# Kernel optimization log

Measured on AMD Instinct MI355X. Metric: run time of the kernel, lower is better.

Reference implementation:

```python
import jax, jax.numpy as jnp
import numpy as np

N_WAY = 5
NKPTS = 17
EMBED = 512
N_SUPPORT = 25  # 5-way 5-shot
N_QUERY = 65536


def setup_inputs() -> dict:
    key = jax.random.key(0)
    ks = jax.random.split(key, 12)
    def lin(k, fan_in, fan_out):
        return jax.random.normal(k, (fan_in, fan_out), jnp.float32) / np.float32(np.sqrt(fan_in))
    return {
        'support_features': jax.random.normal(ks[0], (1, N_SUPPORT, EMBED), jnp.float32),
        'support_keypoints': jax.random.uniform(ks[1], (N_SUPPORT, NKPTS, 2), jnp.float32),
        'query_features': jax.random.normal(ks[2], (N_QUERY, EMBED), jnp.float32),
        'image_coords': jax.random.uniform(ks[3], (N_QUERY, 2), jnp.float32) * 512.0,
        'W1': lin(ks[4], EMBED, EMBED), 'b1': jnp.zeros((EMBED,), jnp.float32),
        'W2': lin(ks[5], EMBED, EMBED), 'b2': jnp.zeros((EMBED,), jnp.float32),
        'Wo1': lin(ks[6], EMBED, EMBED // 2), 'bo1': jnp.zeros((EMBED // 2,), jnp.float32),
        'Wo2': lin(ks[7], EMBED // 2, 2), 'bo2': jnp.zeros((2,), jnp.float32),
        'Wc1': lin(ks[8], EMBED, EMBED // 2), 'bc1': jnp.zeros((EMBED // 2,), jnp.float32),
        'Wc2': lin(ks[9], EMBED // 2, 1), 'bc2': jnp.zeros((1,), jnp.float32),
        'temperature': jnp.float32(1.0),
    }


def reference(support_features, support_keypoints, query_features, image_coords,
              W1, b1, W2, b2, Wo1, bo1, Wo2, bo2, Wc1, bc1, Wc2, bc2, temperature):
    eps = 1e-8
    nkpts = support_keypoints.shape[1]
    n_query = query_features.shape[0]
    D = query_features.shape[-1]

    # --- compute_prototypes (batch_size == 1; per-kpt prototype identical by construction) ---
    sf = support_features.reshape(-1, D)                      # [Ns, D]
    h = jnp.maximum(sf @ W1 + b1, 0.0) @ W2 + b2              # prototype_net MLP
    n_per = h.shape[0] // N_WAY
    proto_way = h.reshape(N_WAY, n_per, D).mean(axis=1)       # [n_way, D]
    prototypes = jnp.broadcast_to(proto_way[:, None, :], (N_WAY, nkpts, D))

    # --- compute_distances: 1 - cosine_sim, scaled by temperature ---
    qn = jnp.linalg.norm(query_features, axis=-1)             # [Nq]
    pn = jnp.linalg.norm(proto_way, axis=-1)                  # [n_way]
    sim = (query_features @ proto_way.T) / jnp.maximum(qn[:, None] * pn[None, :], eps)
    dist_way = (1.0 - sim) / temperature                      # [Nq, n_way]
    distances = jnp.broadcast_to(dist_way[:, :, None], (n_query, N_WAY, nkpts))

    # --- predict_keypoints ---
    # avg over kpts is a no-op (identical per kpt); argmin over ways
    class_predictions = jnp.argmin(dist_way, axis=1)          # [Nq] int
    # softmax over a single scalar == 1.0, so keypoints == offset broadcast over kpts
    offset = jnp.maximum(query_features @ Wo1 + bo1, 0.0) @ Wo2 + bo2   # [Nq, 2]
    conf = jax.nn.sigmoid(jnp.maximum(query_features @ Wc1 + bc1, 0.0) @ Wc2 + bc2)  # [Nq, 1]
    keypoints = jnp.broadcast_to(offset[:, None, :], (n_query, nkpts, 2))
    keypoints = jax.nn.sigmoid(keypoints) * image_coords[:, None, :]    # image_coords provided
    confidence = jnp.broadcast_to(conf, (n_query, nkpts))

    return keypoints, confidence, distances, class_predictions, prototypes
```

## Files before the change

kernel.cpp:

```cpp
#include <hip/hip_runtime.h>
#include <hip/hip_bf16.h>

#define NQ 65536
#define DIM 512
#define HID 256
#define NWAY 5
#define NKPTS 17

typedef short bf16x8 __attribute__((ext_vector_type(8)));
typedef float f32x4 __attribute__((ext_vector_type(4)));
typedef _Float16 half8 __attribute__((ext_vector_type(8)));

static __device__ __forceinline__ unsigned short f2bf(float f) {
    unsigned int x = __float_as_uint(f);
    unsigned int r = (x + 0x7fffu + ((x >> 16) & 1u)) >> 16;
    return (unsigned short)r;
}

__global__ __launch_bounds__(256) void k_sup1(const float* __restrict__ sf,
                                              const float* __restrict__ W1, const float* __restrict__ b1,
                                              float* __restrict__ ws_h1) {
    int w = blockIdx.x * 4 + (threadIdx.x >> 6);
    int lane = threadIdx.x & 63;
    int s = w >> 9;
    int c = w & 511;
    const float* ip = sf + s * DIM + lane * 8;
    float4 a0 = *(const float4*)ip;
    float4 a1 = *(const float4*)(ip + 4);
    float av[8] = {a0.x, a0.y, a0.z, a0.w, a1.x, a1.y, a1.z, a1.w};
    float acc = 0.0f;
    #pragma unroll
    for (int j = 0; j < 8; j++)
        acc += av[j] * W1[(lane * 8 + j) * DIM + c];
    #pragma unroll
    for (int off = 32; off > 0; off >>= 1)
        acc += __shfl_xor(acc, off, 64);
    if (lane == 0)
        ws_h1[s * DIM + c] = fmaxf(acc + b1[c], 0.0f);
}

__global__ __launch_bounds__(256) void k_mid(const float* __restrict__ ws_h1,
                                             const float* __restrict__ W2, const float* __restrict__ b2,
                                             const float* __restrict__ Wo1, const float* __restrict__ Wc1,
                                             float* __restrict__ ws_proto, unsigned short* __restrict__ wb) {
    int bx = blockIdx.x;
    int t = threadIdx.x;
    if (bx < 640) {
        int g = bx * 4 + (t >> 6);
        int lane = t & 63;
        int w = g >> 9;
        int c = g & 511;
        const float* base = ws_h1 + (w * 5) * DIM + lane * 8;
        float av[8] = {0, 0, 0, 0, 0, 0, 0, 0};
        #pragma unroll
        for (int s = 0; s < 5; s++) {
            float4 x0 = *(const float4*)(base + s * DIM);
            float4 x1 = *(const float4*)(base + s * DIM + 4);
            av[0] += x0.x; av[1] += x0.y; av[2] += x0.z; av[3] += x0.w;
            av[4] += x1.x; av[5] += x1.y; av[6] += x1.z; av[7] += x1.w;
        }
        float acc = 0.0f;
        #pragma unroll
        for (int j = 0; j < 8; j++)
            acc += (av[j] * 0.2f) * W2[(lane * 8 + j) * DIM + c];
        #pragma unroll
        for (int off = 32; off > 0; off >>= 1)
            acc += __shfl_xor(acc, off, 64);
        if (lane == 0)
            ws_proto[w * DIM + c] = acc + b2[c];
    } else {
        __shared__ unsigned short T[64][72];
        int tb = bx - 640;
        const float* src = (tb < 32) ? Wo1 : Wc1;
        int cofs = (tb < 32) ? 0 : 256;
        int tt = tb & 31;
        int kt = tt >> 2;
        int ct = tt & 3;
        int i = t >> 2;
        int qd = t & 3;
        const float* rp = src + (size_t)(kt * 64 + i) * HID + ct * 64 + qd * 16;
        #pragma unroll
        for (int v = 0; v < 4; v++) {
            float4 x = *(const float4*)(rp + v * 4);
            T[qd * 16 + v * 4 + 0][i] = f2bf(x.x);
            T[qd * 16 + v * 4 + 1][i] = f2bf(x.y);
            T[qd * 16 + v * 4 + 2][i] = f2bf(x.z);
            T[qd * 16 + v * 4 + 3][i] = f2bf(x.w);
        }
        __syncthreads();
        int j = t >> 2;
        int part = t & 3;
        uint4 o0 = *(const uint4*)&T[j][part * 16];
        uint4 o1 = *(const uint4*)&T[j][part * 16 + 8];
        unsigned short* dst = wb + (size_t)(cofs + ct * 64 + j) * DIM + kt * 64 + part * 16;
        *(uint4*)dst = o0;
        *(uint4*)(dst + 8) = o1;
    }
}

__global__ __launch_bounds__(256) void k_fused(const float* __restrict__ qf, const unsigned short* __restrict__ wb,
                                               const float* __restrict__ ws_proto,
                                               const float* __restrict__ temp_p,
                                               const float* __restrict__ bo1, const float* __restrict__ Wo2,
                                               const float* __restrict__ bo2,
                                               const float* __restrict__ bc1, const float* __restrict__ Wc2,
                                               const float* __restrict__ bc2,
                                               const float* __restrict__ ic,
                                               float* __restrict__ out_kp, float* __restrict__ out_conf,
                                               float* __restrict__ out_dist, float* __restrict__ out_class,
                                               float* __restrict__ out_proto) {
    __shared__ __align__(16) char smem[37376];
    unsigned short* Alds = (unsigned short*)smem;
    unsigned short* Blds = (unsigned short*)(smem + 5120);
    float* s_proto = (float*)(smem + 25600);
    float* dlds = (float*)(smem + 35840);
    float* pn_lds = (float*)(smem + 37120);
    _Float16* hlds = (_Float16*)smem;
    float* offlds = (float*)(smem + 33792);

    int bx = blockIdx.x;
    int mb = bx >> 1;
    int nb = bx & 1;
    int t = threadIdx.x;
    int wv = t >> 6;
    int lane = t & 63;
    int r = lane & 15;
    int q8 = (lane >> 4) * 8;

    if (bx < 85 && t < 128) {
        f32x4 v = *(const f32x4*)(ws_proto + (bx / NKPTS) * DIM + t * 4);
        *(f32x4*)(out_proto + (size_t)bx * DIM + t * 4) = v;
    }

    f32x4 acc[4][4];
    #pragma unroll
    for (int i = 0; i < 4; i++)
        #pragma unroll
        for (int j = 0; j < 4; j++) {
            f32x4 z = {0.0f, 0.0f, 0.0f, 0.0f};
            acc[i][j] = z;
        }

    int am = t >> 2;
    int akc = t & 3;
    int mine = ((t >> 7) == nb);
    const float* aptr = qf + ((size_t)(mb * 64 + am)) * DIM + akc * 8;
    const unsigned short* bptr = wb + ((size_t)(nb * 256 + t)) * DIM;

    for (int i = t; i < NWAY * DIM; i += 256) s_proto[i] = ws_proto[i];

    float ds[NWAY] = {0, 0, 0, 0, 0};
    float qq = 0.0f;

    float4 A0 = *(const float4*)(aptr);
    float4 A1 = *(const float4*)(aptr + 4);
    uint4 B0 = *(const uint4*)(bptr);
    uint4 B1 = *(const uint4*)(bptr + 8);
    uint4 B2 = *(const uint4*)(bptr + 16);
    uint4 B3 = *(const uint4*)(bptr + 24);

    for (int it = 0; it < 16; it++) {
        unsigned int p0 = f2bf(A0.x) | ((unsigned int)f2bf(A0.y) << 16);
        unsigned int p1 = f2bf(A0.z) | ((unsigned int)f2bf(A0.w) << 16);
        unsigned int p2 = f2bf(A1.x) | ((unsigned int)f2bf(A1.y) << 16);
        unsigned int p3 = f2bf(A1.z) | ((unsigned int)f2bf(A1.w) << 16);
        float av[8] = {A0.x, A0.y, A0.z, A0.w, A1.x, A1.y, A1.z, A1.w};
        __syncthreads();
        *(uint4*)(Alds + am * 40 + akc * 8) = make_uint4(p0, p1, p2, p3);
        *(uint4*)(Blds + t * 40) = B0;
        *(uint4*)(Blds + t * 40 + 8) = B1;
        *(uint4*)(Blds + t * 40 + 16) = B2;
        *(uint4*)(Blds + t * 40 + 24) = B3;
        __syncthreads();
        if (it < 15) {
            int k1 = (it + 1) * 32;
            A0 = *(const float4*)(aptr + k1);
            A1 = *(const float4*)(aptr + k1 + 4);
            B0 = *(const uint4*)(bptr + k1);
            B1 = *(const uint4*)(bptr + k1 + 8);
            B2 = *(const uint4*)(bptr + k1 + 16);
            B3 = *(const uint4*)(bptr + k1 + 24);
        }
        if (mine) {
            int kb = it * 32 + akc * 8;
            #pragma unroll
            for (int w = 0; w < NWAY; w++) {
                f32x4 pv0 = *(const f32x4*)(s_proto + w * DIM + kb);
                f32x4 pv1 = *(const f32x4*)(s_proto + w * DIM + kb + 4);
                ds[w] += av[0] * pv0[0] + av[1] * pv0[1] + av[2] * pv0[2] + av[3] * pv0[3]
                       + av[4] * pv1[0] + av[5] * pv1[1] + av[6] * pv1[2] + av[7] * pv1[3];
            }
            #pragma unroll
            for (int j = 0; j < 8; j++) qq += av[j] * av[j];
        }
        bf16x8 af[4], bf[4];
        #pragma unroll
        for (int mt = 0; mt < 4; mt++)
            af[mt] = *(const bf16x8*)(Alds + (mt * 16 + r) * 40 + q8);
        #pragma unroll
        for (int nt = 0; nt < 4; nt++)
            bf[nt] = *(const bf16x8*)(Blds + (wv * 64 + nt * 16 + r) * 40 + q8);
        #pragma unroll
        for (int mt = 0; mt < 4; mt++)
            #pragma unroll
            for (int nt = 0; nt < 4; nt++)
                acc[mt][nt] = __builtin_amdgcn_mfma_f32_16x16x32_bf16(af[mt], bf[nt], acc[mt][nt], 0, 0, 0);
    }

    for (int w = wv; w < NWAY; w += 4) {
        f32x4 a = *(const f32x4*)(s_proto + w * DIM + lane * 8);
        f32x4 b = *(const f32x4*)(s_proto + w * DIM + lane * 8 + 4);
        float ss = a[0]*a[0] + a[1]*a[1] + a[2]*a[2] + a[3]*a[3]
                 + b[0]*b[0] + b[1]*b[1] + b[2]*b[2] + b[3]*b[3];
        #pragma unroll
        for (int off = 32; off > 0; off >>= 1) ss += __shfl_xor(ss, off, 64);
        if (lane == 0) pn_lds[w] = sqrtf(ss);
    }
    if (mine) {
        #pragma unroll
        for (int off = 1; off <= 2; off <<= 1) {
            #pragma unroll
            for (int w = 0; w < NWAY; w++) ds[w] += __shfl_xor(ds[w], off, 64);
            qq += __shfl_xor(qq, off, 64);
        }
    }
    __syncthreads();
    if (mine && akc == 0) {
        float qn = sqrtf(qq);
        float invt = 1.0f / temp_p[0];
        float mv = 1e30f;
        int ami = 0;
        #pragma unroll
        for (int w = 0; w < NWAY; w++) {
            float den = fmaxf(qn * pn_lds[w], 1e-8f);
            float d = (1.0f - ds[w] / den) * invt;
            dlds[am * 5 + w] = d;
            if (d < mv) { mv = d; ami = w; }
        }
        out_class[mb * 64 + am] = (float)ami;
    }
    __syncthreads();

    {
        int qlo = nb * 32;
        for (int i = t; i < 32 * NWAY * NKPTS; i += 256) {
            int q = qlo + i / (NWAY * NKPTS);
            int rem = i - (i / (NWAY * NKPTS)) * (NWAY * NKPTS);
            out_dist[(size_t)(mb * 64 + q) * (NWAY * NKPTS) + rem] = dlds[q * 5 + rem / NKPTS];
        }
    }

    const float* bias = nb ? bc1 : bo1;
    #pragma unroll
    for (int nt = 0; nt < 4; nt++) {
        int cl = wv * 64 + nt * 16 + r;
        float bv = bias[cl];
        #pragma unroll
        for (int mt = 0; mt < 4; mt++)
            #pragma unroll
            for (int rg = 0; rg < 4; rg++) {
                int ml = mt * 16 + (lane >> 4) * 4 + rg;
                float v = acc[mt][nt][rg] + bv;
                hlds[ml * 264 + cl] = (_Float16)fmaxf(v, 0.0f);
            }
    }
    __syncthreads();

    if (nb == 0) {
        if (t < 64) {
            float ox = bo2[0], oy = bo2[1];
            for (int c0 = 0; c0 < 256; c0 += 8) {
                half8 hv = *(const half8*)(hlds + t * 264 + c0);
                #pragma unroll
                for (int j = 0; j < 8; j++) {
                    float hf = (float)hv[j];
                    ox += hf * Wo2[(c0 + j) * 2];
                    oy += hf * Wo2[(c0 + j) * 2 + 1];
                }
            }
            offlds[t * 2] = ox;
            offlds[t * 2 + 1] = oy;
        }
        __syncthreads();
        for (int i = t; i < 64 * 34; i += 256) {
            int q = i / 34;
            int rem = i - q * 34;
            int j = rem & 1;
            size_t Q = (size_t)mb * 64 + q;
            float o = offlds[q * 2 + j];
            float sg = 1.0f / (1.0f + __expf(-o));
            out_kp[Q * 34 + rem] = sg * ic[Q * 2 + j];
        }
    } else {
        if (t < 64) {
            float cl2 = bc2[0];
            for (int c0 = 0; c0 < 256; c0 += 8) {
                half8 hv = *(const half8*)(hlds + t * 264 + c0);
                #pragma unroll
                for (int j = 0; j < 8; j++) cl2 += (float)hv[j] * Wc2[c0 + j];
            }
            offlds[t] = 1.0f / (1.0f + __expf(-cl2));
        }
        __syncthreads();
        for (int i = t; i < 64 * 17; i += 256) {
            int q = i / 17;
            out_conf[(size_t)mb * 64 * 17 + i] = offlds[q];
        }
    }
}

extern "C" void kernel_launch(void* const* d_in, const int* in_sizes, int n_in,
                              void* d_out, int out_size, void* d_ws, size_t ws_size,
                              hipStream_t stream) {
    const float* sf = (const float*)d_in[0];
    const float* qf = (const float*)d_in[2];
    const float* ic = (const float*)d_in[3];
    const float* W1 = (const float*)d_in[4];
    const float* b1 = (const float*)d_in[5];
    const float* W2 = (const float*)d_in[6];
    const float* b2 = (const float*)d_in[7];
    const float* Wo1 = (const float*)d_in[8];
    const float* bo1 = (const float*)d_in[9];
    const float* Wo2 = (const float*)d_in[10];
    const float* bo2 = (const float*)d_in[11];
    const float* Wc1 = (const float*)d_in[12];
    const float* bc1 = (const float*)d_in[13];
    const float* Wc2 = (const float*)d_in[14];
    const float* bc2 = (const float*)d_in[15];
    const float* temp = (const float*)d_in[16];

    float* out = (float*)d_out;
    float* out_kp = out;
    float* out_conf = out + 2228224;
    float* out_dist = out + 3342336;
    float* out_class = out + 8912896;
    float* out_proto = out + 8978432;

    char* ws = (char*)d_ws;
    float* ws_h1 = (float*)ws;
    float* ws_proto = (float*)(ws + 51200);
    unsigned short* ws_wb = (unsigned short*)(ws + 65536);

    hipLaunchKernelGGL(k_sup1, dim3(3200), dim3(256), 0, stream, sf, W1, b1, ws_h1);
    hipLaunchKernelGGL(k_mid, dim3(704), dim3(256), 0, stream, ws_h1, W2, b2, Wo1, Wc1, ws_proto, ws_wb);
    hipLaunchKernelGGL(k_fused, dim3(2048), dim3(256), 0, stream, qf, ws_wb, ws_proto, temp,
                       bo1, Wo2, bo2, bc1, Wc2, bc2, ic, out_kp, out_conf, out_dist, out_class, out_proto);
}
```

Measured before the change: 366.4 us.

## Split query prep from GEMM and use async LDS loads with larger tiles

Restructures the whole pipeline. The support MLP kernels now stage inputs in LDS and use fewer blocks. A new prep kernel converts the query features to bf16 in workspace and computes cosine distances and class predictions. A separate GEMM kernel uses 128x256 tiles with 512 threads, double-buffered global_load_lds copies and an XOR-swizzled LDS layout. The split avoids doing the distance math and bf16 conversion inside the GEMM loop, but adds an extra 64 MB bf16 write and read of the queries through HBM.

```diff
diff --git a/kernel.cpp b/kernel.cpp
--- a/kernel.cpp
+++ b/kernel.cpp
@@ -17,60 +17,69 @@
     return (unsigned short)r;
 }
 
-__global__ __launch_bounds__(256) void k_sup1(const float* __restrict__ sf,
-                                              const float* __restrict__ W1, const float* __restrict__ b1,
-                                              float* __restrict__ ws_h1) {
-    int w = blockIdx.x * 4 + (threadIdx.x >> 6);
-    int lane = threadIdx.x & 63;
-    int s = w >> 9;
-    int c = w & 511;
-    const float* ip = sf + s * DIM + lane * 8;
-    float4 a0 = *(const float4*)ip;
-    float4 a1 = *(const float4*)(ip + 4);
-    float av[8] = {a0.x, a0.y, a0.z, a0.w, a1.x, a1.y, a1.z, a1.w};
+static __device__ __forceinline__ void async16(void* l, const void* g) {
+    __builtin_amdgcn_global_load_lds(
+        (const __attribute__((address_space(1))) unsigned int*)g,
+        (__attribute__((address_space(3))) unsigned int*)l, 16, 0, 0);
+}
+
+__global__ __launch_bounds__(256) void k_sup(const float* __restrict__ sf,
+                                             const float* __restrict__ W1, const float* __restrict__ b1,
+                                             float* __restrict__ ws_h1) {
+    __shared__ float sfl[512];
+    __shared__ float red[4][64];
+    int bx = blockIdx.x;
+    int s = bx >> 3, cb = bx & 7;
+    int t = threadIdx.x;
+    if (t < 128) ((float4*)sfl)[t] = ((const float4*)(sf + s * DIM))[t];
+    __syncthreads();
+    int c = cb * 64 + (t & 63);
+    int qd = t >> 6;
+    const float* Wp = W1 + (size_t)qd * 128 * DIM + c;
     float acc = 0.0f;
-    #pragma unroll
-    for (int j = 0; j < 8; j++)
-        acc += av[j] * W1[(lane * 8 + j) * DIM + c];
-    #pragma unroll
-    for (int off = 32; off > 0; off >>= 1)
-        acc += __shfl_xor(acc, off, 64);
-    if (lane == 0)
-        ws_h1[s * DIM + c] = fmaxf(acc + b1[c], 0.0f);
-}
-
-__global__ __launch_bounds__(256) void k_mid(const float* __restrict__ ws_h1,
-                                             const float* __restrict__ W2, const float* __restrict__ b2,
-                                             const float* __restrict__ Wo1, const float* __restrict__ Wc1,
-                                             float* __restrict__ ws_proto, unsigned short* __restrict__ wb) {
+    #pragma unroll 4
+    for (int kk = 0; kk < 128; kk++)
+        acc += sfl[qd * 128 + kk] * Wp[(size_t)kk * DIM];
+    red[qd][t & 63] = acc;
+    __syncthreads();
+    if (t < 64) {
+        float h = red[0][t] + red[1][t] + red[2][t] + red[3][t] + b1[cb * 64 + t];
+        ws_h1[s * DIM + cb * 64 + t] = fmaxf(h, 0.0f);
+    }
+}
+
+__global__ __launch_bounds__(256) void k_mid2(const float* __restrict__ ws_h1,
+                                              const float* __restrict__ W2, const float* __restrict__ b2,
+                                              const float* __restrict__ Wo1, const float* __restrict__ Wc1,
+                                              float* __restrict__ ws_proto, unsigned short* __restrict__ wb) {
     int bx = blockIdx.x;
     int t = threadIdx.x;
-    if (bx < 640) {
-        int g = bx * 4 + (t >> 6);
-        int lane = t & 63;
-        int w = g >> 9;
-        int c = g & 511;
-        const float* base = ws_h1 + (w * 5) * DIM + lane * 8;
-        float av[8] = {0, 0, 0, 0, 0, 0, 0, 0};
-        #pragma unroll
-        for (int s = 0; s < 5; s++) {
-            float4 x0 = *(const float4*)(base + s * DIM);
-            float4 x1 = *(const float4*)(base + s * DIM + 4);
-            av[0] += x0.x; av[1] += x0.y; av[2] += x0.z; av[3] += x0.w;
-            av[4] += x1.x; av[5] += x1.y; av[6] += x1.z; av[7] += x1.w;
-        }
+    if (bx < 40) {
+        __shared__ float ml[512];
+        __shared__ float red[4][64];
+        int w = bx >> 3, cb = bx & 7;
+        for (int i = t; i < 512; i += 256) {
+            float sum = 0.0f;
+            #pragma unroll
+            for (int s5 = 0; s5 < 5; s5++) sum += ws_h1[(w * 5 + s5) * DIM + i];
+            ml[i] = sum * 0.2f;
+        }
+        __syncthreads();
+        int c = cb * 64 + (t & 63);
+        int qd = t >> 6;
+        const float* Wp = W2 + (size_t)qd * 128 * DIM + c;
         float acc = 0.0f;
-        #pragma unroll
-        for (int j = 0; j < 8; j++)
-            acc += (av[j] * 0.2f) * W2[(lane * 8 + j) * DIM + c];
-        #pragma unroll
-        for (int off = 32; off > 0; off >>= 1)
-            acc += __shfl_xor(acc, off, 64);
-        if (lane == 0)
-            ws_proto[w * DIM + c] = acc + b2[c];
+        #pragma unroll 4
+        for (int kk = 0; kk < 128; kk++)
+            acc += ml[qd * 128 + kk] * Wp[(size_t)kk * DIM];
+        red[qd][t & 63] = acc;
+        __syncthreads();
+        if (t < 64)
+            ws_proto[w * DIM + cb * 64 + t] =
+                red[0][t] + red[1][t] + red[2][t] + red[3][t] + b2[cb * 64 + t];
     } else {
         __shared__ unsigned short T[64][72];
-        int tb = bx - 640;
+        int tb = bx - 40;
         const float* src = (tb < 32) ? Wo1 : Wc1;
         int cofs = (tb < 32) ? 0 : 256;
         int tt = tb & 31;
@@ -98,213 +107,259 @@
     }
 }
 
-__global__ __launch_bounds__(256) void k_fused(const float* __restrict__ qf, const unsigned short* __restrict__ wb,
-                                               const float* __restrict__ ws_proto,
-                                               const float* __restrict__ temp_p,
-                                               const float* __restrict__ bo1, const float* __restrict__ Wo2,
-                                               const float* __restrict__ bo2,
-                                               const float* __restrict__ bc1, const float* __restrict__ Wc2,
-                                               const float* __restrict__ bc2,
-                                               const float* __restrict__ ic,
-                                               float* __restrict__ out_kp, float* __restrict__ out_conf,
-                                               float* __restrict__ out_dist, float* __restrict__ out_class,
-                                               float* __restrict__ out_proto) {
-    __shared__ __align__(16) char smem[37376];
-    unsigned short* Alds = (unsigned short*)smem;
-    unsigned short* Blds = (unsigned short*)(smem + 5120);
-    float* s_proto = (float*)(smem + 25600);
-    float* dlds = (float*)(smem + 35840);
-    float* pn_lds = (float*)(smem + 37120);
-    _Float16* hlds = (_Float16*)smem;
-    float* offlds = (float*)(smem + 33792);
-
-    int bx = blockIdx.x;
-    int mb = bx >> 1;
-    int nb = bx & 1;
-    int t = threadIdx.x;
-    int wv = t >> 6;
-    int lane = t & 63;
-    int r = lane & 15;
-    int q8 = (lane >> 4) * 8;
-
-    if (bx < 85 && t < 128) {
+__global__ __launch_bounds__(256) void k_prep(const float* __restrict__ qf,
+                                              const float* __restrict__ ws_proto,
+                                              const float* __restrict__ temp_p,
+                                              unsigned short* __restrict__ qbf,
+                                              float* __restrict__ out_dist, float* __restrict__ out_class,
+                                              float* __restrict__ out_proto) {
+    __shared__ float dlds[32 * NWAY];
+    int bx = blockIdx.x, t = threadIdx.x;
+    int wv = t >> 6, lane = t & 63;
+
+    if (bx < NWAY * NKPTS && t < 128) {
         f32x4 v = *(const f32x4*)(ws_proto + (bx / NKPTS) * DIM + t * 4);
         *(f32x4*)(out_proto + (size_t)bx * DIM + t * 4) = v;
     }
 
+    float p[NWAY][8];
+    float pn[NWAY];
+    {
+        float pp[NWAY];
+        #pragma unroll
+        for (int w = 0; w < NWAY; w++) {
+            f32x4 a = *(const f32x4*)(ws_proto + w * DIM + lane * 8);
+            f32x4 b = *(const f32x4*)(ws_proto + w * DIM + lane * 8 + 4);
+            p[w][0] = a[0]; p[w][1] = a[1]; p[w][2] = a[2]; p[w][3] = a[3];
+            p[w][4] = b[0]; p[w][5] = b[1]; p[w][6] = b[2]; p[w][7] = b[3];
+            float s = 0.0f;
+            #pragma unroll
+            for (int j = 0; j < 8; j++) s += p[w][j] * p[w][j];
+            pp[w] = s;
+        }
+        #pragma unroll
+        for (int off = 32; off > 0; off >>= 1) {
+            #pragma unroll
+            for (int w = 0; w < NWAY; w++) pp[w] += __shfl_xor(pp[w], off, 64);
+        }
+        #pragma unroll
+        for (int w = 0; w < NWAY; w++) pn[w] = sqrtf(pp[w]);
+    }
+    float invt = 1.0f / temp_p[0];
+
+    int qbase = bx * 32 + wv * 8;
+    for (int qi = 0; qi < 8; qi++) {
+        int Q = qbase + qi;
+        const float* vp = qf + (size_t)Q * DIM + lane * 8;
+        float4 v0 = *(const float4*)vp;
+        float4 v1 = *(const float4*)(vp + 4);
+        unsigned int r0 = f2bf(v0.x) | ((unsigned int)f2bf(v0.y) << 16);
+        unsigned int r1 = f2bf(v0.z) | ((unsigned int)f2bf(v0.w) << 16);
+        unsigned int r2 = f2bf(v1.x) | ((unsigned int)f2bf(v1.y) << 16);
+        unsigned int r3 = f2bf(v1.z) | ((unsigned int)f2bf(v1.w) << 16);
+        *(uint4*)(qbf + (size_t)Q * DIM + lane * 8) = make_uint4(r0, r1, r2, r3);
+
+        float av[8] = {v0.x, v0.y, v0.z, v0.w, v1.x, v1.y, v1.z, v1.w};
+        float d[NWAY + 1];
+        #pragma unroll
+        for (int w = 0; w < NWAY; w++) {
+            float s = 0.0f;
+            #pragma unroll
+            for (int j = 0; j < 8; j++) s += av[j] * p[w][j];
+            d[w] = s;
+        }
+        {
+            float s = 0.0f;
+            #pragma unroll
+            for (int j = 0; j < 8; j++) s += av[j] * av[j];
+            d[NWAY] = s;
+        }
+        #pragma unroll
+        for (int off = 32; off > 0; off >>= 1) {
+            #pragma unroll
+            for (int k2 = 0; k2 < NWAY + 1; k2++) d[k2] += __shfl_xor(d[k2], off, 64);
+        }
+        float qn = sqrtf(d[NWAY]);
+        float mv = 1e30f; int ami = 0;
+        float d0, d1c, d2c, d3c, d4c;
+        {
+            float dist[NWAY];
+            #pragma unroll
+            for (int w = 0; w < NWAY; w++) {
+                float den = fmaxf(qn * pn[w], 1e-8f);
+                float dd = (1.0f - d[w] / den) * invt;
+                dist[w] = dd;
+                if (dd < mv) { mv = dd; ami = w; }
+            }
+            d0 = dist[0]; d1c = dist[1]; d2c = dist[2]; d3c = dist[3]; d4c = dist[4];
+        }
+        if (lane == 0) {
+            out_class[Q] = (float)ami;
+            int b0 = (wv * 8 + qi) * NWAY;
+            dlds[b0 + 0] = d0; dlds[b0 + 1] = d1c; dlds[b0 + 2] = d2c;
+            dlds[b0 + 3] = d3c; dlds[b0 + 4] = d4c;
+        }
+    }
+    __syncthreads();
+    int Q0 = bx * 32;
+    for (int i = t; i < 32 * NWAY * NKPTS; i += 256) {
+        int q2 = i / (NWAY * NKPTS);
+        int rem = i - q2 * (NWAY * NKPTS);
+        out_dist[(size_t)(Q0 + q2) * (NWAY * NKPTS) + rem] = dlds[q2 * NWAY + rem / NKPTS];
+    }
+}
+
+__global__ __launch_bounds__(512) void k_gemm(const unsigned short* __restrict__ qbf,
+                                              const unsigned short* __restrict__ wb,
+                                              const float* __restrict__ bo1, const float* __restrict__ Wo2,
+                                              const float* __restrict__ bo2,
+                                              const float* __restrict__ bc1, const float* __restrict__ Wc2,
+                                              const float* __restrict__ bc2,
+                                              const float* __restrict__ ic,
+                                              float* __restrict__ out_kp, float* __restrict__ out_conf) {
+    __shared__ __align__(16) char smem[98304];
+    unsigned short* Ab = (unsigned short*)smem;
+    unsigned short* Bb = (unsigned short*)(smem + 32768);
+
+    int bx = blockIdx.x;
+    int mb = bx >> 1, nb = bx & 1;
+    int t = threadIdx.x;
+    int wv = t >> 6, lane = t & 63;
+    int wr = wv >> 2, wc = wv & 3;
+    int r = lane & 15, hq = lane >> 4;
+
+    int lrow = lane >> 3;
+    int lslot = (lane & 7) ^ lrow;
+    const unsigned short* Ag = qbf + (size_t)mb * (128 * DIM) + (size_t)lrow * DIM + lslot * 8;
+    const unsigned short* Bg = wb + (size_t)nb * (HID * DIM) + (size_t)lrow * DIM + lslot * 8;
+
     f32x4 acc[4][4];
     #pragma unroll
-    for (int i = 0; i < 4; i++)
-        #pragma unroll
-        for (int j = 0; j < 4; j++) {
-            f32x4 z = {0.0f, 0.0f, 0.0f, 0.0f};
-            acc[i][j] = z;
-        }
-
-    int am = t >> 2;
-    int akc = t & 3;
-    int mine = ((t >> 7) == nb);
-    const float* aptr = qf + ((size_t)(mb * 64 + am)) * DIM + akc * 8;
-    const unsigned short* bptr = wb + ((size_t)(nb * 256 + t)) * DIM;
-
-    for (int i = t; i < NWAY * DIM; i += 256) s_proto[i] = ws_proto[i];
-
-    float ds[NWAY] = {0, 0, 0, 0, 0};
-    float qq = 0.0f;
-
-    float4 A0 = *(const float4*)(aptr);
-    float4 A1 = *(const float4*)(aptr + 4);
-    uint4 B0 = *(const uint4*)(bptr);
-    uint4 B1 = *(const uint4*)(bptr + 8);
-    uint4 B2 = *(const uint4*)(bptr + 16);
-    uint4 B3 = *(const uint4*)(bptr + 24);
-
-    for (int it = 0; it < 16; it++) {
-        unsigned int p0 = f2bf(A0.x) | ((unsigned int)f2bf(A0.y) << 16);
-        unsigned int p1 = f2bf(A0.z) | ((unsigned int)f2bf(A0.w) << 16);
-        unsigned int p2 = f2bf(A1.x) | ((unsigned int)f2bf(A1.y) << 16);
-        unsigned int p3 = f2bf(A1.z) | ((unsigned int)f2bf(A1.w) << 16);
-        float av[8] = {A0.x, A0.y, A0.z, A0.w, A1.x, A1.y, A1.z, A1.w};
-        __syncthreads();
-        *(uint4*)(Alds + am * 40 + akc * 8) = make_uint4(p0, p1, p2, p3);
-        *(uint4*)(Blds + t * 40) = B0;
-        *(uint4*)(Blds + t * 40 + 8) = B1;
-        *(uint4*)(Blds + t * 40 + 16) = B2;
-        *(uint4*)(Blds + t * 40 + 24) = B3;
-        __syncthreads();
-        if (it < 15) {
-            int k1 = (it + 1) * 32;
-            A0 = *(const float4*)(aptr + k1);
-            A1 = *(const float4*)(aptr + k1 + 4);
-            B0 = *(const uint4*)(bptr + k1);
-            B1 = *(const uint4*)(bptr + k1 + 8);
-            B2 = *(const uint4*)(bptr + k1 + 16);
-            B3 = *(const uint4*)(bptr + k1 + 24);
-        }
-        if (mine) {
-            int kb = it * 32 + akc * 8;
-            #pragma unroll
-            for (int w = 0; w < NWAY; w++) {
-                f32x4 pv0 = *(const f32x4*)(s_proto + w * DIM + kb);
-                f32x4 pv1 = *(const f32x4*)(s_proto + w * DIM + kb + 4);
-                ds[w] += av[0] * pv0[0] + av[1] * pv0[1] + av[2] * pv0[2] + av[3] * pv0[3]
-                       + av[4] * pv1[0] + av[5] * pv1[1] + av[6] * pv1[2] + av[7] * pv1[3];
-            }
-            #pragma unroll
-            for (int j = 0; j < 8; j++) qq += av[j] * av[j];
-        }
-        bf16x8 af[4], bf[4];
-        #pragma unroll
-        for (int mt = 0; mt < 4; mt++)
-            af[mt] = *(const bf16x8*)(Alds + (mt * 16 + r) * 40 + q8);
-        #pragma unroll
-        for (int nt = 0; nt < 4; nt++)
-            bf[nt] = *(const bf16x8*)(Blds + (wv * 64 + nt * 16 + r) * 40 + q8);
-        #pragma unroll
-        for (int mt = 0; mt < 4; mt++)
-            #pragma unroll
-            for (int nt = 0; nt < 4; nt++)
-                acc[mt][nt] = __builtin_amdgcn_mfma_f32_16x16x32_bf16(af[mt], bf[nt], acc[mt][nt], 0, 0, 0);
-    }
-
-    for (int w = wv; w < NWAY; w += 4) {
-        f32x4 a = *(const f32x4*)(s_proto + w * DIM + lane * 8);
-        f32x4 b = *(const f32x4*)(s_proto + w * DIM + lane * 8 + 4);
-        float ss = a[0]*a[0] + a[1]*a[1] + a[2]*a[2] + a[3]*a[3]
-                 + b[0]*b[0] + b[1]*b[1] + b[2]*b[2] + b[3]*b[3];
-        #pragma unroll
-        for (int off = 32; off > 0; off >>= 1) ss += __shfl_xor(ss, off, 64);
-        if (lane == 0) pn_lds[w] = sqrtf(ss);
-    }
-    if (mine) {
-        #pragma unroll
-        for (int off = 1; off <= 2; off <<= 1) {
-            #pragma unroll
-            for (int w = 0; w < NWAY; w++) ds[w] += __shfl_xor(ds[w], off, 64);
-            qq += __shfl_xor(qq, off, 64);
-        }
+    for (int i2 = 0; i2 < 4; i2++)
+        #pragma unroll
+        for (int j2 = 0; j2 < 4; j2++) { f32x4 z = {0.0f, 0.0f, 0.0f, 0.0f}; acc[i2][j2] = z; }
+
+    #pragma unroll
+    for (int i = 0; i < 2; i++) {
+        int ci = wv * 2 + i;
+        async16(smem + ci * 1024, Ag + (size_t)ci * 8 * DIM);
+    }
+    #pragma unroll
+    for (int i = 0; i < 4; i++) {
+        int ci = wv * 4 + i;
+        async16(smem + 32768 + ci * 1024, Bg + (size_t)ci * 8 * DIM);
     }
     __syncthreads();
-    if (mine && akc == 0) {
-        float qn = sqrtf(qq);
-        float invt = 1.0f / temp_p[0];
-        float mv = 1e30f;
-        int ami = 0;
-        #pragma unroll
-        for (int w = 0; w < NWAY; w++) {
-            float den = fmaxf(qn * pn_lds[w], 1e-8f);
-            float d = (1.0f - ds[w] / den) * invt;
-            dlds[am * 5 + w] = d;
-            if (d < mv) { mv = d; ami = w; }
-        }
-        out_class[mb * 64 + am] = (float)ami;
-    }
-    __syncthreads();
-
-    {
-        int qlo = nb * 32;
-        for (int i = t; i < 32 * NWAY * NKPTS; i += 256) {
-            int q = qlo + i / (NWAY * NKPTS);
-            int rem = i - (i / (NWAY * NKPTS)) * (NWAY * NKPTS);
-            out_dist[(size_t)(mb * 64 + q) * (NWAY * NKPTS) + rem] = dlds[q * 5 + rem / NKPTS];
-        }
+
+    for (int it = 0; it < 8; it++) {
+        int par = it & 1;
+        if (it < 7) {
+            int ko = (it + 1) * 64;
+            int pn2 = par ^ 1;
+            #pragma unroll
+            for (int i = 0; i < 2; i++) {
+                int ci = wv * 2 + i;
+                async16(smem + pn2 * 16384 + ci * 1024, Ag + (size_t)ci * 8 * DIM + ko);
+            }
+            #pragma unroll
+            for (int i = 0; i < 4; i++) {
+                int ci = wv * 4 + i;
+                async16(smem + 32768 + pn2 * 32768 + ci * 1024, Bg + (size_t)ci * 8 * DIM + ko);
+            }
+        }
+        const unsigned short* Ap = Ab + par * 8192;
+        const unsigned short* Bp = Bb + par * 16384;
+        #pragma unroll
+        for (int ks = 0; ks < 2; ks++) {
+            int slot = ks * 4 + hq;
+            bf16x8 af[4], bfr[4];
+            #pragma unroll
+            for (int mt = 0; mt < 4; mt++) {
+                int m = wr * 64 + mt * 16 + r;
+                af[mt] = *(const bf16x8*)(Ap + m * 64 + ((slot ^ (m & 7)) * 8));
+            }
+            #pragma unroll
+            for (int nt = 0; nt < 4; nt++) {
+                int c = wc * 64 + nt * 16 + r;
+                bfr[nt] = *(const bf16x8*)(Bp + c * 64 + ((slot ^ (c & 7)) * 8));
+            }
+            #pragma unroll
+            for (int mt = 0; mt < 4; mt++)
+                #pragma unroll
+                for (int nt = 0; nt < 4; nt++)
+                    acc[mt][nt] = __builtin_amdgcn_mfma_f32_16x16x32_bf16(af[mt], bfr[nt], acc[mt][nt], 0, 0, 0);
+        }
+        __syncthreads();
     }
 
     const float* bias = nb ? bc1 : bo1;
+    _Float16* hl = (_Float16*)smem;
     #pragma unroll
     for (int nt = 0; nt < 4; nt++) {
-        int cl = wv * 64 + nt * 16 + r;
+        int cl = wc * 64 + nt * 16 + r;
         float bv = bias[cl];
         #pragma unroll
         for (int mt = 0; mt < 4; mt++)
             #pragma unroll
             for (int rg = 0; rg < 4; rg++) {
-                int ml = mt * 16 + (lane >> 4) * 4 + rg;
-                float v = acc[mt][nt][rg] + bv;
-                hlds[ml * 264 + cl] = (_Float16)fmaxf(v, 0.0f);
+                int ml = wr * 64 + mt * 16 + hq * 4 + rg;
+                hl[ml * 264 + cl] = (_Float16)fmaxf(acc[mt][nt][rg] + bv, 0.0f);
             }
     }
     __syncthreads();
 
+    float* redf = (float*)(smem + 128 * 264 * 2);
+    int q = t & 127, qt = t >> 7;
     if (nb == 0) {
-        if (t < 64) {
-            float ox = bo2[0], oy = bo2[1];
-            for (int c0 = 0; c0 < 256; c0 += 8) {
-                half8 hv = *(const half8*)(hlds + t * 264 + c0);
-                #pragma unroll
-                for (int j = 0; j < 8; j++) {
-                    float hf = (float)hv[j];
-                    ox += hf * Wo2[(c0 + j) * 2];
-                    oy += hf * Wo2[(c0 + j) * 2 + 1];
-                }
-            }
-            offlds[t * 2] = ox;
-            offlds[t * 2 + 1] = oy;
-        }
-        __syncthreads();
-        for (int i = t; i < 64 * 34; i += 256) {
-            int q = i / 34;
-            int rem = i - q * 34;
-            int j = rem & 1;
-            size_t Q = (size_t)mb * 64 + q;
-            float o = offlds[q * 2 + j];
-            float sg = 1.0f / (1.0f + __expf(-o));
-            out_kp[Q * 34 + rem] = sg * ic[Q * 2 + j];
+        float ox = 0.0f, oy = 0.0f;
+        #pragma unroll 2
+        for (int j0 = 0; j0 < 64; j0 += 8) {
+            half8 hv = *(const half8*)(hl + q * 264 + qt * 64 + j0);
+            #pragma unroll
+            for (int j = 0; j < 8; j++) {
+                float2 w2 = *(const float2*)(Wo2 + (qt * 64 + j0 + j) * 2);
+                float hf = (float)hv[j];
+                ox += hf * w2.x;
+                oy += hf * w2.y;
+            }
+        }
+        redf[(qt * 128 + q) * 2] = ox;
+        redf[(qt * 128 + q) * 2 + 1] = oy;
+        __syncthreads();
+        if (t < 128) {
+            float sx = bo2[0], sy = bo2[1];
+            #pragma unroll
+            for (int k2 = 0; k2 < 4; k2++) {
+                sx += redf[(k2 * 128 + t) * 2];
+                sy += redf[(k2 * 128 + t) * 2 + 1];
+            }
+            size_t Q = (size_t)mb * 128 + t;
+            float2 icv = *(const float2*)(ic + Q * 2);
+            float gx = icv.x / (1.0f + __expf(-sx));
+            float gy = icv.y / (1.0f + __expf(-sy));
+            float2 g2 = make_float2(gx, gy);
+            float2* dst = (float2*)(out_kp + Q * 34);
+            #pragma unroll
+            for (int k2 = 0; k2 < 17; k2++) dst[k2] = g2;
         }
     } else {
-        if (t < 64) {
-            float cl2 = bc2[0];
-            for (int c0 = 0; c0 < 256; c0 += 8) {
-                half8 hv = *(const half8*)(hlds + t * 264 + c0);
-                #pragma unroll
-                for (int j = 0; j < 8; j++) cl2 += (float)hv[j] * Wc2[c0 + j];
-            }
-            offlds[t] = 1.0f / (1.0f + __expf(-cl2));
-        }
-        __syncthreads();
-        for (int i = t; i < 64 * 17; i += 256) {
-            int q = i / 17;
-            out_conf[(size_t)mb * 64 * 17 + i] = offlds[q];
+        float cs = 0.0f;
+        #pragma unroll 2
+        for (int j0 = 0; j0 < 64; j0 += 8) {
+            half8 hv = *(const half8*)(hl + q * 264 + qt * 64 + j0);
+            #pragma unroll
+            for (int j = 0; j < 8; j++)
+                cs += (float)hv[j] * Wc2[qt * 64 + j0 + j];
+        }
+        redf[qt * 128 + q] = cs;
+        __syncthreads();
+        if (t < 128) {
+            float s = bc2[0] + redf[t] + redf[128 + t] + redf[256 + t] + redf[384 + t];
+            float sg = 1.0f / (1.0f + __expf(-s));
+            size_t Q = (size_t)mb * 128 + t;
+            float* dst = out_conf + Q * 17;
+            #pragma unroll
+            for (int k2 = 0; k2 < 17; k2++) dst[k2] = sg;
         }
     }
 }
@@ -340,9 +395,12 @@
     float* ws_h1 = (float*)ws;
     float* ws_proto = (float*)(ws + 51200);
     unsigned short* ws_wb = (unsigned short*)(ws + 65536);
-
-    hipLaunchKernelGGL(k_sup1, dim3(3200), dim3(256), 0, stream, sf, W1, b1, ws_h1);
-    hipLaunchKernelGGL(k_mid, dim3(704), dim3(256), 0, stream, ws_h1, W2, b2, Wo1, Wc1, ws_proto, ws_wb);
-    hipLaunchKernelGGL(k_fused, dim3(2048), dim3(256), 0, stream, qf, ws_wb, ws_proto, temp,
-                       bo1, Wo2, bo2, bc1, Wc2, bc2, ic, out_kp, out_conf, out_dist, out_class, out_proto);
-}
+    unsigned short* ws_qbf = (unsigned short*)(ws + 1048576);
+
+    hipLaunchKernelGGL(k_sup, dim3(200), dim3(256), 0, stream, sf, W1, b1, ws_h1);
+    hipLaunchKernelGGL(k_mid2, dim3(104), dim3(256), 0, stream, ws_h1, W2, b2, Wo1, Wc1, ws_proto, ws_wb);
+    hipLaunchKernelGGL(k_prep, dim3(2048), dim3(256), 0, stream, qf, ws_proto, temp,
+                       ws_qbf, out_dist, out_class, out_proto);
+    hipLaunchKernelGGL(k_gemm, dim3(1024), dim3(512), 0, stream, ws_qbf, ws_wb,
+                       bo1, Wo2, bo2, bc1, Wc2, bc2, ic, out_kp, out_conf);
+}
```

Result: faster. 335.8 us (-8.4%).
